# Optimization experiments

Hardware: AMD Instinct MI355X
Metric: run time of the kernel (lower is better)

The kernel has to match this reference:

```python
import jax, jax.numpy as jnp
import numpy as np

N, M, D = 4096, 8192, 512

def setup_inputs() -> dict:
    key = jax.random.key(0)
    k1, k2, k3, k4 = jax.random.split(key, 4)
    X = jax.random.normal(k1, (N, D), dtype=jnp.float32)
    SV = jax.random.normal(k2, (M, D), dtype=jnp.float32)
    DC = jax.random.normal(k3, (1, M), dtype=jnp.float32)
    IC = jax.random.normal(k4, (1,), dtype=jnp.float32)
    gamma = jnp.float32(1.0 / D)
    return {"X": X, "SV": SV, "DC": DC, "IC": IC, "gamma": gamma}

def reference(X, SV, DC, IC, gamma):
    # Squared pairwise L2 distances via GEMM expansion (same math as
    # ||SV - x||^2 without materializing the [N, M, D] broadcast tensor):
    # d2[n, m] = ||x_n||^2 + ||sv_m||^2 - 2 * x_n . sv_m
    x2 = jnp.sum(X * X, axis=1)          # [N]
    sv2 = jnp.sum(SV * SV, axis=1)       # [M]
    cross = jnp.einsum("nd,md->nm", X, SV)  # [N, M]
    d2 = jnp.maximum(x2[:, None] + sv2[None, :] - 2.0 * cross, 0.0)
    k = jnp.exp(-gamma * d2)             # RBF kernel values [N, M]
    # Weighted reduction over support vectors + intercept -> decision values [N]
    return jnp.sum(k * DC, axis=1) + IC
```

## Files before the change

### kernel.cpp

```cpp
#include <hip/hip_runtime.h>
#include <stdint.h>

#define NN 4096
#define MM 8192
#define DD 512
#define KT 8

typedef __bf16 bf16x8 __attribute__((ext_vector_type(8)));
typedef __bf16 bf16x4 __attribute__((ext_vector_type(4)));
typedef float f32x4 __attribute__((ext_vector_type(4)));
typedef float f32x16 __attribute__((ext_vector_type(16)));

__device__ __forceinline__ void load_lds16(const void* g, void* l) {
  __builtin_amdgcn_global_load_lds(
      (const __attribute__((address_space(1))) unsigned int*)g,
      (__attribute__((address_space(3))) unsigned int*)l, 16, 0, 0);
}

template <int CTRL>
__device__ __forceinline__ float dpp_radd(float x) {
  int xi = __float_as_int(x);
  int mv = __builtin_amdgcn_update_dpp(xi, xi, CTRL, 0xF, 0xF, false);
  return x + __int_as_float(mv);
}
__device__ __forceinline__ float swz_add_xor16(float x) {
  int sv = __builtin_amdgcn_ds_swizzle(__float_as_int(x), 0x401F);
  return x + __int_as_float(sv);
}

__global__ __launch_bounds__(256) void convert_norm_kernel(
    const float* __restrict__ X, const float* __restrict__ SV,
    __bf16* __restrict__ Xb, __bf16* __restrict__ SVb,
    float* __restrict__ x2, float* __restrict__ sv2,
    float* __restrict__ out, const float* __restrict__ IC) {
  int wid = blockIdx.x * 4 + (threadIdx.x >> 6);
  int lane = threadIdx.x & 63;
  const float* src;
  __bf16* dst;
  float* nrm;
  if (wid < NN) {
    src = X + (size_t)wid * DD;
    dst = Xb + (size_t)wid * DD;
    nrm = x2 + wid;
    if (lane == 0) out[wid] = IC[0];
  } else {
    int r = wid - NN;
    src = SV + (size_t)r * DD;
    dst = SVb + (size_t)r * DD;
    nrm = sv2 + r;
  }
  const f32x4* s = (const f32x4*)src;
  f32x4 a = s[lane];
  f32x4 b = s[lane + 64];
  float sum = a.x * a.x + a.y * a.y + a.z * a.z + a.w * a.w +
              b.x * b.x + b.y * b.y + b.z * b.z + b.w * b.w;
  bf16x4 ca = {(__bf16)a.x, (__bf16)a.y, (__bf16)a.z, (__bf16)a.w};
  bf16x4 cb = {(__bf16)b.x, (__bf16)b.y, (__bf16)b.z, (__bf16)b.w};
  *(bf16x4*)(dst + 4 * lane) = ca;
  *(bf16x4*)(dst + 256 + 4 * lane) = cb;
#pragma unroll
  for (int m = 32; m >= 1; m >>= 1) sum += __shfl_xor(sum, m, 64);
  if (lane == 0) *nrm = sum;
}

__global__ __launch_bounds__(256, 4) void rbf_gemm_kernel(
    const bf16x8* __restrict__ Xb, const bf16x8* __restrict__ SVb,
    const float* __restrict__ x2, const float* __restrict__ sv2,
    const float* __restrict__ DC, const float* __restrict__ gamma_p,
    float* __restrict__ out) {
  __shared__ bf16x8 As[1024];
  __shared__ bf16x8 Bs[1024];

  const int t = threadIdx.x;
  const int lane = t & 63;
  const int wave = t >> 6;

  const int id = blockIdx.y * gridDim.x + blockIdx.x;
  const int xcd = id & 7;
  const int idx = id >> 3;
  const int bn = (xcd & 1) * 16 + (idx & 15);
  const int bm = (xcd >> 1) * 16 + (idx >> 4);
  const int n0 = bn * 128;
  const int m0 = bm * 128;

  const int wave_m = wave & 1;
  const int wave_n = wave >> 1;
  const int l31 = lane & 31;
  const int lhi = lane >> 5;

  const int srow = t >> 3;
  const int sslot = t & 7;

  f32x16 acc[2][2];
#pragma unroll
  for (int i = 0; i < 2; ++i)
#pragma unroll
    for (int j = 0; j < 2; ++j)
#pragma unroll
      for (int r = 0; r < 16; ++r) acc[i][j][r] = 0.0f;

  for (int kt = 0; kt < KT; ++kt) {
#pragma unroll
    for (int it = 0; it < 4; ++it) {
      const int c = it * 256 + t;
      const int row = it * 32 + srow;
      const int kg = sslot ^ (row & 7);
      load_lds16(Xb + (size_t)(n0 + row) * 64 + kt * 8 + kg, &As[c]);
      load_lds16(SVb + (size_t)(m0 + row) * 64 + kt * 8 + kg, &Bs[c]);
    }
    __syncthreads();
#pragma unroll
    for (int ks = 0; ks < 4; ++ks) {
      const int kc = ks * 2 + lhi;
      const int sw = kc ^ (l31 & 7);
      const int ra = (wave_n * 64 + l31) * 8;
      const int rb = (wave_m * 64 + l31) * 8;
      bf16x8 af0 = As[ra + sw];
      bf16x8 af1 = As[ra + 256 + sw];
      bf16x8 bf0 = Bs[rb + sw];
      bf16x8 bf1 = Bs[rb + 256 + sw];
      acc[0][0] = __builtin_amdgcn_mfma_f32_32x32x16_bf16(af0, bf0, acc[0][0], 0, 0, 0);
      acc[0][1] = __builtin_amdgcn_mfma_f32_32x32x16_bf16(af0, bf1, acc[0][1], 0, 0, 0);
      acc[1][0] = __builtin_amdgcn_mfma_f32_32x32x16_bf16(af1, bf0, acc[1][0], 0, 0, 0);
      acc[1][1] = __builtin_amdgcn_mfma_f32_32x32x16_bf16(af1, bf1, acc[1][1], 0, 0, 0);
    }
    __syncthreads();
  }

  const float g = gamma_p[0];
  const float c2 = g * 1.4426950408889634f;

  float sv2v[2], dcv[2];
  const int colb = m0 + wave_m * 64 + l31;
  sv2v[0] = sv2[colb];
  dcv[0] = DC[colb];
  sv2v[1] = sv2[colb + 32];
  dcv[1] = DC[colb + 32];

#pragma unroll
  for (int i = 0; i < 2; ++i) {
    const int rowb = n0 + wave_n * 64 + i * 32 + 4 * lhi;
    float val[16];
#pragma unroll
    for (int g4 = 0; g4 < 4; ++g4) {
      f32x4 xv = *(const f32x4*)(x2 + rowb + 8 * g4);
#pragma unroll
      for (int r2 = 0; r2 < 4; ++r2) {
        const int reg = g4 * 4 + r2;
        float v = 0.0f;
#pragma unroll
        for (int j = 0; j < 2; ++j) {
          float d2 = xv[r2] + sv2v[j] - 2.0f * acc[i][j][reg];
          d2 = fmaxf(d2, 0.0f);
          v += exp2f(-c2 * d2) * dcv[j];
        }
        val[reg] = v;
      }
    }
#pragma unroll
    for (int reg = 0; reg < 16; ++reg) {
      float v = val[reg];
      v = dpp_radd<0x121>(v);
      v = dpp_radd<0x122>(v);
      v = dpp_radd<0x124>(v);
      v = dpp_radd<0x128>(v);
      val[reg] = swz_add_xor16(v);
    }
    if (l31 == 0) {
#pragma unroll
      for (int g4 = 0; g4 < 4; ++g4)
#pragma unroll
        for (int r2 = 0; r2 < 4; ++r2)
          atomicAdd(&out[rowb + 8 * g4 + r2], val[g4 * 4 + r2]);
    }
  }
}

extern "C" void kernel_launch(void* const* d_in, const int* in_sizes, int n_in,
                              void* d_out, int out_size, void* d_ws, size_t ws_size,
                              hipStream_t stream) {
  const float* X = (const float*)d_in[0];
  const float* SV = (const float*)d_in[1];
  const float* DC = (const float*)d_in[2];
  const float* IC = (const float*)d_in[3];
  const float* gamma = (const float*)d_in[4];
  float* out = (float*)d_out;

  char* ws = (char*)d_ws;
  __bf16* Xb = (__bf16*)ws;
  __bf16* SVb = (__bf16*)(ws + (size_t)NN * DD * 2);
  float* x2 = (float*)(ws + (size_t)(NN + MM) * DD * 2);
  float* sv2 = x2 + NN;

  convert_norm_kernel<<<(NN + MM) / 4, 256, 0, stream>>>(X, SV, Xb, SVb, x2, sv2, out, IC);
  dim3 grid(NN / 128, MM / 128);
  rbf_gemm_kernel<<<grid, 256, 0, stream>>>((const bf16x8*)Xb, (const bf16x8*)SVb,
                                            x2, sv2, DC, gamma, out);
}
```

Before: 132.1 us.

## Widen GEMM tile to 128x256 and fold RBF epilogue into FMAs

Doubles the per-block M tile from 128 to 256 support vectors, so each wave computes a 64x128 sub-tile with eight MFMA accumulators instead of four. This raises operand reuse per LDS read, and halves the X-tile reloads and output atomics per row. The epilogue is also rewritten to compute the exponent directly with fused multiply-adds and a min clamp. The cost is more accumulator registers and double the B-tile LDS, with occupancy lowered to 3 blocks per CU and half as many blocks in the grid.

```diff
diff --git a/kernel.cpp b/kernel.cpp
--- a/kernel.cpp
+++ b/kernel.cpp
@@ -63,13 +63,13 @@
   if (lane == 0) *nrm = sum;
 }
 
-__global__ __launch_bounds__(256, 4) void rbf_gemm_kernel(
+__global__ __launch_bounds__(256, 3) void rbf_gemm_kernel(
     const bf16x8* __restrict__ Xb, const bf16x8* __restrict__ SVb,
     const float* __restrict__ x2, const float* __restrict__ sv2,
     const float* __restrict__ DC, const float* __restrict__ gamma_p,
     float* __restrict__ out) {
   __shared__ bf16x8 As[1024];
-  __shared__ bf16x8 Bs[1024];
+  __shared__ bf16x8 Bs[2048];
 
   const int t = threadIdx.x;
   const int lane = t & 63;
@@ -79,23 +79,23 @@
   const int xcd = id & 7;
   const int idx = id >> 3;
   const int bn = (xcd & 1) * 16 + (idx & 15);
-  const int bm = (xcd >> 1) * 16 + (idx >> 4);
+  const int bm = (xcd >> 1) * 8 + (idx >> 4);
   const int n0 = bn * 128;
-  const int m0 = bm * 128;
-
-  const int wave_m = wave & 1;
-  const int wave_n = wave >> 1;
+  const int m0 = bm * 256;
+
+  const int wave_n = wave & 1;
+  const int wave_m = wave >> 1;
   const int l31 = lane & 31;
   const int lhi = lane >> 5;
 
   const int srow = t >> 3;
   const int sslot = t & 7;
 
-  f32x16 acc[2][2];
+  f32x16 acc[2][4];
 #pragma unroll
   for (int i = 0; i < 2; ++i)
 #pragma unroll
-    for (int j = 0; j < 2; ++j)
+    for (int j = 0; j < 4; ++j)
 #pragma unroll
       for (int r = 0; r < 16; ++r) acc[i][j][r] = 0.0f;
 
@@ -106,36 +106,50 @@
       const int row = it * 32 + srow;
       const int kg = sslot ^ (row & 7);
       load_lds16(Xb + (size_t)(n0 + row) * 64 + kt * 8 + kg, &As[c]);
+    }
+#pragma unroll
+    for (int it = 0; it < 8; ++it) {
+      const int c = it * 256 + t;
+      const int row = it * 32 + srow;
+      const int kg = sslot ^ (row & 7);
       load_lds16(SVb + (size_t)(m0 + row) * 64 + kt * 8 + kg, &Bs[c]);
     }
     __syncthreads();
+    const int ra = (wave_n * 64 + l31) * 8;
+    const int rb = (wave_m * 128 + l31) * 8;
 #pragma unroll
     for (int ks = 0; ks < 4; ++ks) {
-      const int kc = ks * 2 + lhi;
-      const int sw = kc ^ (l31 & 7);
-      const int ra = (wave_n * 64 + l31) * 8;
-      const int rb = (wave_m * 64 + l31) * 8;
+      const int sw = (ks * 2 + lhi) ^ (l31 & 7);
       bf16x8 af0 = As[ra + sw];
       bf16x8 af1 = As[ra + 256 + sw];
       bf16x8 bf0 = Bs[rb + sw];
       bf16x8 bf1 = Bs[rb + 256 + sw];
+      bf16x8 bf2 = Bs[rb + 512 + sw];
+      bf16x8 bf3 = Bs[rb + 768 + sw];
       acc[0][0] = __builtin_amdgcn_mfma_f32_32x32x16_bf16(af0, bf0, acc[0][0], 0, 0, 0);
       acc[0][1] = __builtin_amdgcn_mfma_f32_32x32x16_bf16(af0, bf1, acc[0][1], 0, 0, 0);
+      acc[0][2] = __builtin_amdgcn_mfma_f32_32x32x16_bf16(af0, bf2, acc[0][2], 0, 0, 0);
+      acc[0][3] = __builtin_amdgcn_mfma_f32_32x32x16_bf16(af0, bf3, acc[0][3], 0, 0, 0);
       acc[1][0] = __builtin_amdgcn_mfma_f32_32x32x16_bf16(af1, bf0, acc[1][0], 0, 0, 0);
       acc[1][1] = __builtin_amdgcn_mfma_f32_32x32x16_bf16(af1, bf1, acc[1][1], 0, 0, 0);
+      acc[1][2] = __builtin_amdgcn_mfma_f32_32x32x16_bf16(af1, bf2, acc[1][2], 0, 0, 0);
+      acc[1][3] = __builtin_amdgcn_mfma_f32_32x32x16_bf16(af1, bf3, acc[1][3], 0, 0, 0);
     }
     __syncthreads();
   }
 
   const float g = gamma_p[0];
   const float c2 = g * 1.4426950408889634f;
-
-  float sv2v[2], dcv[2];
-  const int colb = m0 + wave_m * 64 + l31;
-  sv2v[0] = sv2[colb];
-  dcv[0] = DC[colb];
-  sv2v[1] = sv2[colb + 32];
-  dcv[1] = DC[colb + 32];
+  const float t2 = 2.0f * c2;
+
+  float sv2v[4], dcv[4], nsv[4];
+  const int colb = m0 + wave_m * 128 + l31;
+#pragma unroll
+  for (int j = 0; j < 4; ++j) {
+    sv2v[j] = sv2[colb + 32 * j];
+    dcv[j] = DC[colb + 32 * j];
+    nsv[j] = -c2 * sv2v[j];
+  }
 
 #pragma unroll
   for (int i = 0; i < 2; ++i) {
@@ -149,10 +163,10 @@
         const int reg = g4 * 4 + r2;
         float v = 0.0f;
 #pragma unroll
-        for (int j = 0; j < 2; ++j) {
-          float d2 = xv[r2] + sv2v[j] - 2.0f * acc[i][j][reg];
-          d2 = fmaxf(d2, 0.0f);
-          v += exp2f(-c2 * d2) * dcv[j];
+        for (int j = 0; j < 4; ++j) {
+          float e = fmaf(t2, acc[i][j][reg], fmaf(-c2, xv[r2], nsv[j]));
+          e = fminf(e, 0.0f);
+          v = fmaf(exp2f(e), dcv[j], v);
         }
         val[reg] = v;
       }
@@ -193,7 +207,7 @@
   float* sv2 = x2 + NN;
 
   convert_norm_kernel<<<(NN + MM) / 4, 256, 0, stream>>>(X, SV, Xb, SVb, x2, sv2, out, IC);
-  dim3 grid(NN / 128, MM / 128);
+  dim3 grid(NN / 128, MM / 256);
   rbf_gemm_kernel<<<grid, 256, 0, stream>>>((const bf16x8*)Xb, (const bf16x8*)SVb,
                                             x2, sv2, DC, gamma, out);
 }
```

Result: slower. 150.7 us (+14.1%).

## Double-buffer LDS with K-step 32 and fold epilogue into FMAs

Applied to the files above, without the earlier changes.

Each K tile shrinks from 64 to 32 elements and LDS is split into two buffers, so the global-to-LDS load for the next tile is issued before computing the current one. This halves the barriers per step of work and overlaps memory latency with MFMA work, at the cost of more, smaller steps (16 instead of 8) and a new XOR swizzle pattern. The epilogue rewrites the distance and exponent into pre-scaled FMAs with a min clamp, which trims a few ALU ops per element.

```diff
diff --git a/kernel.cpp b/kernel.cpp
--- a/kernel.cpp
+++ b/kernel.cpp
@@ -4,7 +4,6 @@
 #define NN 4096
 #define MM 8192
 #define DD 512
-#define KT 8
 
 typedef __bf16 bf16x8 __attribute__((ext_vector_type(8)));
 typedef __bf16 bf16x4 __attribute__((ext_vector_type(4)));
@@ -88,8 +87,17 @@
   const int l31 = lane & 31;
   const int lhi = lane >> 5;
 
-  const int srow = t >> 3;
-  const int sslot = t & 7;
+  const int srow = t >> 2;
+  const int sslot = t & 3;
+  const int kg = sslot ^ (srow & 3) ^ ((srow >> 3) & 3);
+  const bf16x8* gA0 = Xb + (size_t)(n0 + srow) * 64 + kg;
+  const bf16x8* gA1 = Xb + (size_t)(n0 + srow + 64) * 64 + kg;
+  const bf16x8* gB0 = SVb + (size_t)(m0 + srow) * 64 + kg;
+  const bf16x8* gB1 = SVb + (size_t)(m0 + srow + 64) * 64 + kg;
+
+  const int ra = (wave_n * 64 + l31) * 4;
+  const int rb = (wave_m * 64 + l31) * 4;
+  const int xsw = (l31 & 3) ^ ((l31 >> 3) & 3);
 
   f32x16 acc[2][2];
 #pragma unroll
@@ -99,43 +107,53 @@
 #pragma unroll
       for (int r = 0; r < 16; ++r) acc[i][j][r] = 0.0f;
 
-  for (int kt = 0; kt < KT; ++kt) {
-#pragma unroll
-    for (int it = 0; it < 4; ++it) {
-      const int c = it * 256 + t;
-      const int row = it * 32 + srow;
-      const int kg = sslot ^ (row & 7);
-      load_lds16(Xb + (size_t)(n0 + row) * 64 + kt * 8 + kg, &As[c]);
-      load_lds16(SVb + (size_t)(m0 + row) * 64 + kt * 8 + kg, &Bs[c]);
-    }
-    __syncthreads();
-#pragma unroll
-    for (int ks = 0; ks < 4; ++ks) {
-      const int kc = ks * 2 + lhi;
-      const int sw = kc ^ (l31 & 7);
-      const int ra = (wave_n * 64 + l31) * 8;
-      const int rb = (wave_m * 64 + l31) * 8;
-      bf16x8 af0 = As[ra + sw];
-      bf16x8 af1 = As[ra + 256 + sw];
-      bf16x8 bf0 = Bs[rb + sw];
-      bf16x8 bf1 = Bs[rb + 256 + sw];
+  auto stage = [&](int h, int p) {
+    const int o = h * 4;
+    const int d = p * 512 + t;
+    load_lds16(gA0 + o, &As[d]);
+    load_lds16(gA1 + o, &As[d + 256]);
+    load_lds16(gB0 + o, &Bs[d]);
+    load_lds16(gB1 + o, &Bs[d + 256]);
+  };
+  auto compute = [&](int p) {
+    const bf16x8* Ab = As + p * 512;
+    const bf16x8* Bb = Bs + p * 512;
+#pragma unroll
+    for (int ks = 0; ks < 2; ++ks) {
+      const int sw = (ks * 2 + lhi) ^ xsw;
+      bf16x8 af0 = Ab[ra + sw];
+      bf16x8 af1 = Ab[ra + 128 + sw];
+      bf16x8 bf0 = Bb[rb + sw];
+      bf16x8 bf1 = Bb[rb + 128 + sw];
       acc[0][0] = __builtin_amdgcn_mfma_f32_32x32x16_bf16(af0, bf0, acc[0][0], 0, 0, 0);
       acc[0][1] = __builtin_amdgcn_mfma_f32_32x32x16_bf16(af0, bf1, acc[0][1], 0, 0, 0);
       acc[1][0] = __builtin_amdgcn_mfma_f32_32x32x16_bf16(af1, bf0, acc[1][0], 0, 0, 0);
       acc[1][1] = __builtin_amdgcn_mfma_f32_32x32x16_bf16(af1, bf1, acc[1][1], 0, 0, 0);
     }
+  };
+
+  stage(0, 0);
+  __syncthreads();
+
+  for (int h = 0; h < 15; ++h) {
+    stage(h + 1, (h + 1) & 1);
+    compute(h & 1);
     __syncthreads();
   }
+  compute(1);
 
   const float g = gamma_p[0];
   const float c2 = g * 1.4426950408889634f;
-
-  float sv2v[2], dcv[2];
+  const float t2 = 2.0f * c2;
+
+  float sv2v[2], dcv[2], nsv[2];
   const int colb = m0 + wave_m * 64 + l31;
   sv2v[0] = sv2[colb];
   dcv[0] = DC[colb];
   sv2v[1] = sv2[colb + 32];
   dcv[1] = DC[colb + 32];
+  nsv[0] = -c2 * sv2v[0];
+  nsv[1] = -c2 * sv2v[1];
 
 #pragma unroll
   for (int i = 0; i < 2; ++i) {
@@ -150,9 +168,9 @@
         float v = 0.0f;
 #pragma unroll
         for (int j = 0; j < 2; ++j) {
-          float d2 = xv[r2] + sv2v[j] - 2.0f * acc[i][j][reg];
-          d2 = fmaxf(d2, 0.0f);
-          v += exp2f(-c2 * d2) * dcv[j];
+          float e = fmaf(t2, acc[i][j][reg], fmaf(-c2, xv[r2], nsv[j]));
+          e = fminf(e, 0.0f);
+          v = fmaf(exp2f(e), dcv[j], v);
         }
         val[reg] = v;
       }
```

Measured after the change: 135.1 us. 1.02x slower.

## Split K-tile LDS layout into halves with new swizzle and fold epilogue into FMAs

Applied to the files above, without the earlier changes.

Reorganizes the shared-memory tile so each 64-element K slab is stored as two 32-element halves (4 vectors per row per half), with an XOR swizzle mixing row bits 0-1 and 3-4. This is meant to cut LDS bank conflicts on the MFMA fragment reads. The epilogue is also rewritten to compute the exponent directly with fused multiply-adds, precomputing -c2*sv2 and clamping with fminf. That trims ALU work per element but changes rounding slightly.

```diff
diff --git a/kernel.cpp b/kernel.cpp
--- a/kernel.cpp
+++ b/kernel.cpp
@@ -88,8 +88,12 @@
   const int l31 = lane & 31;
   const int lhi = lane >> 5;
 
-  const int srow = t >> 3;
-  const int sslot = t & 7;
+  const int srow_ = (t >> 2) & 63;
+  const int sslot = t & 3;
+
+  const int ra = (wave_n * 64 + l31) * 4;
+  const int rb = (wave_m * 64 + l31) * 4;
+  const int xsw = (l31 & 3) ^ ((l31 >> 3) & 3);
 
   f32x16 acc[2][2];
 #pragma unroll
@@ -103,8 +107,9 @@
 #pragma unroll
     for (int it = 0; it < 4; ++it) {
       const int c = it * 256 + t;
-      const int row = it * 32 + srow;
-      const int kg = sslot ^ (row & 7);
+      const int half = c >> 9;
+      const int row = (c >> 2) & 127;
+      const int kg = half * 4 + (sslot ^ (row & 3) ^ ((row >> 3) & 3));
       load_lds16(Xb + (size_t)(n0 + row) * 64 + kt * 8 + kg, &As[c]);
       load_lds16(SVb + (size_t)(m0 + row) * 64 + kt * 8 + kg, &Bs[c]);
     }
@@ -112,13 +117,14 @@
 #pragma unroll
     for (int ks = 0; ks < 4; ++ks) {
       const int kc = ks * 2 + lhi;
-      const int sw = kc ^ (l31 & 7);
-      const int ra = (wave_n * 64 + l31) * 8;
-      const int rb = (wave_m * 64 + l31) * 8;
-      bf16x8 af0 = As[ra + sw];
-      bf16x8 af1 = As[ra + 256 + sw];
-      bf16x8 bf0 = Bs[rb + sw];
-      bf16x8 bf1 = Bs[rb + 256 + sw];
+      const int h = ks >> 1;
+      const int sw = (kc & 3) ^ xsw;
+      const bf16x8* Ah = As + h * 512;
+      const bf16x8* Bh = Bs + h * 512;
+      bf16x8 af0 = Ah[ra + sw];
+      bf16x8 af1 = Ah[ra + 128 + sw];
+      bf16x8 bf0 = Bh[rb + sw];
+      bf16x8 bf1 = Bh[rb + 128 + sw];
       acc[0][0] = __builtin_amdgcn_mfma_f32_32x32x16_bf16(af0, bf0, acc[0][0], 0, 0, 0);
       acc[0][1] = __builtin_amdgcn_mfma_f32_32x32x16_bf16(af0, bf1, acc[0][1], 0, 0, 0);
       acc[1][0] = __builtin_amdgcn_mfma_f32_32x32x16_bf16(af1, bf0, acc[1][0], 0, 0, 0);
@@ -129,13 +135,16 @@
 
   const float g = gamma_p[0];
   const float c2 = g * 1.4426950408889634f;
-
-  float sv2v[2], dcv[2];
+  const float t2 = 2.0f * c2;
+
+  float sv2v[2], dcv[2], nsv[2];
   const int colb = m0 + wave_m * 64 + l31;
   sv2v[0] = sv2[colb];
   dcv[0] = DC[colb];
   sv2v[1] = sv2[colb + 32];
   dcv[1] = DC[colb + 32];
+  nsv[0] = -c2 * sv2v[0];
+  nsv[1] = -c2 * sv2v[1];
 
 #pragma unroll
   for (int i = 0; i < 2; ++i) {
@@ -150,9 +159,9 @@
         float v = 0.0f;
 #pragma unroll
         for (int j = 0; j < 2; ++j) {
-          float d2 = xv[r2] + sv2v[j] - 2.0f * acc[i][j][reg];
-          d2 = fmaxf(d2, 0.0f);
-          v += exp2f(-c2 * d2) * dcv[j];
+          float e = fmaf(t2, acc[i][j][reg], fmaf(-c2, xv[r2], nsv[j]));
+          e = fminf(e, 0.0f);
+          v = fmaf(exp2f(e), dcv[j], v);
         }
         val[reg] = v;
       }
```

New measurement: 130.2 us. About the same (-1.4%).
